# Kernel tuning notes

Hardware: AMD Instinct MI355X
Metric: run time of the kernel (lower is better)

## Reference

```python
import jax, jax.numpy as jnp
import numpy as np

B, L, DN, DE, DD, H = 2, 512, 512, 128, 128, 8
DK, DEH, DDH = DN // H, DE // H, DD // H
F = 2 * DK + DEH + 2 * DDH  # per-head concat feature size (176)
SLOPE = 0.2


def _kaiming(key, out_f, in_f):
    bound = np.sqrt(6.0 / ((1.0 + SLOPE ** 2) * in_f))
    return jax.random.uniform(key, (out_f, in_f), minval=-bound, maxval=bound, dtype=jnp.float32)


def lin(x, w, b):
    y = jnp.einsum('...i,oi->...o', x, w)
    return y if b is None else y + b


def setup_inputs() -> dict:
    key = jax.random.key(0)
    ks = jax.random.split(key, 16)
    inp = {
        'node_representation': jax.random.normal(ks[0], (B, L, DN), dtype=jnp.float32),
        'edge_representation': jax.random.normal(ks[1], (B, L, L, DE), dtype=jnp.float32),
        'diff_vec': jax.random.normal(ks[2], (B, L, DD), dtype=jnp.float32),
        'Wn_w': _kaiming(ks[3], DN, DN), 'Wn_b': jnp.zeros((DN,), jnp.float32),
        'We_w': _kaiming(ks[4], DE, DE), 'We_b': jnp.zeros((DE,), jnp.float32),
        'Wd_w': _kaiming(ks[5], DD, DD), 'Wd_b': jnp.zeros((DD,), jnp.float32),
        'Wh_w': _kaiming(ks[6], DK, DK), 'Wh_b': jnp.zeros((DK,), jnp.float32),
        'attn_w': _kaiming(ks[7], 1, F),
        'outn_w': _kaiming(ks[8], DN, DN), 'outn_b': jnp.zeros((DN,), jnp.float32),
        'Wn2_w': _kaiming(ks[9], DN, DN), 'Wn2_b': jnp.zeros((DN,), jnp.float32),
        'We2_w': _kaiming(ks[10], DE, DE), 'We2_b': jnp.zeros((DE,), jnp.float32),
        'Wd2_w': _kaiming(ks[11], DD, DD), 'Wd2_b': jnp.zeros((DD,), jnp.float32),
        'edge_w': _kaiming(ks[12], DEH, F), 'edge_b': jnp.zeros((DEH,), jnp.float32),
        'oute_w': _kaiming(ks[13], DE, DE), 'oute_b': jnp.zeros((DE,), jnp.float32),
    }
    return inp


def reference(node_representation, edge_representation, diff_vec,
              Wn_w, Wn_b, We_w, We_b, Wd_w, Wd_b, Wh_w, Wh_b, attn_w,
              outn_w, outn_b, Wn2_w, Wn2_b, We2_w, We2_b, Wd2_w, Wd2_b,
              edge_w, edge_b, oute_w, oute_b):
    lrelu = lambda x: jax.nn.leaky_relu(x, SLOPE)

    # ---- node update (GAT-style with concat score decomposed per term) ----
    npj = lin(node_representation, Wn_w, Wn_b).reshape(B, L, H, DK)
    epj = lin(edge_representation, We_w, We_b).reshape(B, L, L, H, DEH)
    dpj = lin(diff_vec, Wd_w, Wd_b).reshape(B, L, H, DDH)
    a = attn_w[0]  # concat order: [hi, hj, edge, di, dj]
    a_hi, a_hj = a[:DK], a[DK:2 * DK]
    a_e = a[2 * DK:2 * DK + DEH]
    a_di, a_dj = a[2 * DK + DEH:2 * DK + DEH + DDH], a[-DDH:]
    # scores[b,i,j,h]
    s = (jnp.einsum('blhd,d->blh', npj, a_hi)[:, :, None, :]
         + jnp.einsum('blhd,d->blh', npj, a_hj)[:, None, :, :]
         + jnp.einsum('blmhe,e->blmh', epj, a_e)
         + jnp.einsum('blhd,d->blh', dpj, a_di)[:, :, None, :]
         + jnp.einsum('blhd,d->blh', dpj, a_dj)[:, None, :, :])
    diag = jnp.eye(L, dtype=bool)[None, :, :, None]
    s = jnp.where(diag, -jnp.inf, s)
    probs = jax.nn.softmax(lrelu(s), axis=2)  # softmax over j
    node_wh = lin(npj, Wh_w, Wh_b)  # [B,L,H,DK]
    agg = jnp.einsum('blmh,bmhd->blhd', probs, node_wh)
    new_node = (npj + lrelu(agg)).reshape(B, L, DN)
    new_node = lin(new_node, outn_w, outn_b)

    # ---- edge update (concat-linear decomposed into per-term matmuls) ----
    np2 = lin(new_node, Wn2_w, Wn2_b).reshape(B, L, H, DK)
    ep2 = lin(edge_representation, We2_w, We2_b).reshape(B, L, L, H, DEH)
    dp2 = lin(diff_vec, Wd2_w, Wd2_b).reshape(B, L, H, DDH)
    # edge concat order: [edge, hi, hj, di, dj]
    W_e = edge_w[:, :DEH]
    W_hi = edge_w[:, DEH:DEH + DK]
    W_hj = edge_w[:, DEH + DK:DEH + 2 * DK]
    W_di = edge_w[:, DEH + 2 * DK:DEH + 2 * DK + DDH]
    W_dj = edge_w[:, -DDH:]
    e_out = (jnp.einsum('blmhe,fe->blmhf', ep2, W_e)
             + jnp.einsum('blhd,fd->blhf', np2, W_hi)[:, :, None]
             + jnp.einsum('blhd,fd->blhf', np2, W_hj)[:, None]
             + jnp.einsum('blhd,fd->blhf', dp2, W_di)[:, :, None]
             + jnp.einsum('blhd,fd->blhf', dp2, W_dj)[:, None]
             + edge_b)
    new_edge = lin(e_out.reshape(B, L, L, DE), oute_w, oute_b)
    return new_node, new_edge
```

## Files before the change

kernel.cpp:

```cpp
#include <hip/hip_runtime.h>
#include <hip/hip_bf16.h>

typedef unsigned short u16;
typedef unsigned short u16x8 __attribute__((ext_vector_type(8)));
typedef __bf16 bf16x8 __attribute__((ext_vector_type(8)));
typedef float f32x4 __attribute__((ext_vector_type(4)));

#define LRS 0.2f

__device__ __forceinline__ u16 f2b(float f) {
  __hip_bfloat16 h = __float2bfloat16(f);
  return __builtin_bit_cast(u16, h);
}

template<int K, int O, int KSEG, int R>
__device__ __forceinline__ void gemm_rowsR(const float* xr, const float* W, const float* bias,
                                           float* yl, float* yg, int ygstride) {
  constexpr int KPT = K / KSEG;
  constexpr int OPP = 256 / KSEG;
  const int t = threadIdx.x;
  const int ks = t % KSEG;
  const int oi = t / KSEG;
#pragma unroll
  for (int pass = 0; pass < O / OPP; ++pass) {
    const int o = pass * OPP + oi;
    float a[R];
#pragma unroll
    for (int r = 0; r < R; ++r) a[r] = 0.0f;
    const float* wp = W + (size_t)o * K + ks * KPT;
    const float* xb = xr + ks * KPT;
#pragma unroll 4
    for (int kc = 0; kc < KPT; kc += 4) {
      f32x4 w4 = *(const f32x4*)(wp + kc);
#pragma unroll
      for (int r = 0; r < R; ++r) {
        f32x4 x = *(const f32x4*)(xb + r * K + kc);
#pragma unroll
        for (int j = 0; j < 4; ++j) a[r] += x[j] * w4[j];
      }
    }
#pragma unroll
    for (int d = 1; d < KSEG; d <<= 1)
#pragma unroll
      for (int r = 0; r < R; ++r) a[r] += __shfl_xor(a[r], d, 64);
    if (ks == 0) {
      float bv = bias ? bias[o] : 0.0f;
#pragma unroll
      for (int r = 0; r < R; ++r) {
        float v = a[r] + bv;
        if (yl) yl[r * O + o] = v;
        if (yg) yg[(size_t)r * ygstride + o] = v;
      }
    }
  }
}

__global__ __launch_bounds__(256) void kW1(const float* We_w, const float* We_b, const float* attn,
                                           const float* We2_w, const float* We2_b,
                                           const float* edge_w, const float* edge_b,
                                           float* Mfull, u16* vb, float* cbe, float* sconst) {
  int gid = blockIdx.x * 256 + threadIdx.x;
  if (gid < 16384) {
    int hf = gid >> 7, c = gid & 127;
    int h = hf >> 4, fo = hf & 15;
    float s = 0;
    for (int e = 0; e < 16; ++e)
      s += edge_w[fo * 176 + e] * We2_w[(h * 16 + e) * 128 + c];
    Mfull[hf * 128 + c] = s;
  } else if (gid < 16384 + 2048) {
    int idx = gid - 16384;
    int c = idx >> 4, hc = idx & 15;
    float s = 0;
    if (hc < 8)
      for (int e = 0; e < 16; ++e)
        s += We_w[(hc * 16 + e) * 128 + c] * attn[128 + e];
    vb[c * 16 + hc] = f2b(s);
  } else if (gid < 18432 + 128) {
    int hf = gid - 18432;
    int h = hf >> 4, fo = hf & 15;
    float s = edge_b[fo];
    for (int e = 0; e < 16; ++e)
      s += We2_b[h * 16 + e] * edge_w[fo * 176 + e];
    cbe[hf] = s;
  } else if (gid < 18560 + 8) {
    int h = gid - 18560;
    float s = 0;
    for (int e = 0; e < 16; ++e)
      s += We_b[h * 16 + e] * attn[128 + e];
    sconst[h] = s;
  }
}

__global__ __launch_bounds__(256) void kW2(const float* oute_w, const float* Mfull, u16* Gb) {
  int gid = blockIdx.x * 256 + threadIdx.x;
  int o = gid >> 7, c = gid & 127;
  float s = 0;
  for (int k = 0; k < 128; ++k)
    s += oute_w[o * 128 + k] * Mfull[k * 128 + c];
  Gb[o * 128 + c] = f2b(s);
}

__global__ __launch_bounds__(256) void kN1(const float* node, const float* diff,
                                           const float* Wn_w, const float* Wn_b,
                                           const float* Wd_w, const float* Wd_b,
                                           const float* Wh_w, const float* Wh_b,
                                           const float* attn, const float* sconst,
                                           float* npj_g, float* nwh_g,
                                           float* srow_g, float* scol_g) {
  __shared__ float nrow[2 * 512], npjl[2 * 512], drow[2 * 128], dpjl[2 * 128];
  const int t = threadIdx.x;
  const int r0 = blockIdx.x * 2;
  *(f32x4*)&nrow[t * 4] = *(const f32x4*)(node + (size_t)r0 * 512 + t * 4);
  if (t < 64) *(f32x4*)&drow[t * 4] = *(const f32x4*)(diff + (size_t)r0 * 128 + t * 4);
  __syncthreads();
  gemm_rowsR<512, 512, 4, 2>(nrow, Wn_w, Wn_b, npjl, npj_g + (size_t)r0 * 512, 512);
  gemm_rowsR<128, 128, 4, 2>(drow, Wd_w, Wd_b, dpjl, nullptr, 0);
  __syncthreads();
  {
    int d = t & 63, hh = t >> 6;
#pragma unroll
    for (int hi = 0; hi < 2; ++hi) {
      int h = hh + hi * 4;
      float wb = Wh_b[d];
      float acc[2] = {wb, wb};
      for (int k = 0; k < 64; ++k) {
        float w = Wh_w[d * 64 + k];
#pragma unroll
        for (int r = 0; r < 2; ++r) acc[r] += npjl[r * 512 + h * 64 + k] * w;
      }
#pragma unroll
      for (int r = 0; r < 2; ++r) nwh_g[(size_t)(r0 + r) * 512 + h * 64 + d] = acc[r];
    }
  }
  if (t < 16) {
    int r = t >> 3, h = t & 7;
    float shi = 0, shj = 0, sdi = 0, sdj = 0;
    for (int d = 0; d < 64; ++d) {
      float x = npjl[r * 512 + h * 64 + d];
      shi += x * attn[d];
      shj += x * attn[64 + d];
    }
    for (int e = 0; e < 16; ++e) {
      float x = dpjl[r * 128 + h * 16 + e];
      sdi += x * attn[144 + e];
      sdj += x * attn[160 + e];
    }
    srow_g[(r0 + r) * 8 + h] = shi + sdi + sconst[h];
    scol_g[(r0 + r) * 8 + h] = shj + sdj;
  }
}

__global__ __launch_bounds__(256) void kA(const float* edge, const float* npj, const float* nwh,
                                          const float* srow, const float* scol,
                                          const u16* vb, float* nnp, u16* abf) {
  __shared__ u16 At[8192];
  __shared__ float sm[4608];
  __shared__ float part[2][512];
  __shared__ float red[256];
  __shared__ float mxh8[8], inv8[8];
  const int bl = blockIdx.x;
  const int b = bl >> 9, l = bl & 511;
  const int t = threadIdx.x;
  const int lane = t & 63, w = t >> 6;
  const int colL = lane & 15, kg = lane >> 4;
  const int h = t & 7, seg = t >> 3;
  const int arow = t >> 2, aseg = t & 3;

  bf16x8 bfr[4];
#pragma unroll
  for (int ks = 0; ks < 4; ++ks) {
    u16x8 u;
#pragma unroll
    for (int j = 0; j < 8; ++j) u[j] = vb[(ks * 32 + kg * 8 + j) * 16 + colL];
    bfr[ks] = __builtin_bit_cast(bf16x8, u);
  }

  for (int tl = 0; tl < 8; ++tl) {
    {
      const float* p = edge + ((size_t)bl * 512 + tl * 64 + arow) * 128 + aseg * 32;
      f32x4 v[8];
#pragma unroll
      for (int q = 0; q < 8; ++q) v[q] = *(const f32x4*)(p + q * 4);
      u16* dst = abf ? abf + ((size_t)bl * 8 + tl) * 8192 : nullptr;
#pragma unroll
      for (int jj = 0; jj < 4; ++jj) {
        u16x8 a8;
#pragma unroll
        for (int j2 = 0; j2 < 4; ++j2) {
          a8[j2]     = f2b(v[2 * jj][j2]);
          a8[4 + j2] = f2b(v[2 * jj + 1][j2]);
        }
        int cu = aseg * 4 + jj;
        int su = arow * 16 + (cu ^ (arow & 7));
        *(u16x8*)(At + su * 8) = a8;
        if (dst) *(u16x8*)(dst + su * 8) = a8;
      }
    }
    __syncthreads();
    f32x4 acc = {0, 0, 0, 0};
#pragma unroll
    for (int ks = 0; ks < 4; ++ks) {
      int cu = ks * 4 + kg;
      int lrow = w * 16 + colL;
      bf16x8 af = *(bf16x8*)(At + (lrow * 16 + (cu ^ (lrow & 7))) * 8);
      acc = __builtin_amdgcn_mfma_f32_16x16x32_bf16(af, bfr[ks], acc, 0, 0, 0);
    }
    if (colL < 8) {
#pragma unroll
      for (int r = 0; r < 4; ++r) {
        int m = tl * 64 + w * 16 + kg * 4 + r;
        sm[m * 9 + colL] = acc[r];
      }
    }
    __syncthreads();
  }

  const float srh2 = srow[(size_t)bl * 8 + h];
  float mx = -__builtin_inff();
#pragma unroll 4
  for (int i = 0; i < 16; ++i) {
    int m = seg * 16 + i;
    float sv = sm[m * 9 + h] + srh2 + scol[((size_t)b * 512 + m) * 8 + h];
    sv = (m == l) ? -__builtin_inff() : (sv >= 0.0f ? sv : LRS * sv);
    sm[m * 9 + h] = sv;
    mx = fmaxf(mx, sv);
  }
  red[t] = mx;
  __syncthreads();
  if (t < 8) {
    float m2 = -__builtin_inff();
    for (int sg = 0; sg < 32; ++sg) m2 = fmaxf(m2, red[sg * 8 + t]);
    mxh8[t] = m2;
  }
  __syncthreads();
  float mh = mxh8[h];
  float smv = 0;
#pragma unroll 4
  for (int i = 0; i < 16; ++i) {
    int m = seg * 16 + i;
    float p = __expf(sm[m * 9 + h] - mh);
    sm[m * 9 + h] = p;
    smv += p;
  }
  red[t] = smv;
  __syncthreads();
  if (t < 8) {
    float s2 = 0;
    for (int sg = 0; sg < 32; ++sg) s2 += red[sg * 8 + t];
    inv8[t] = 1.0f / s2;
  }
  __syncthreads();
  const int half = t >> 7, oq = t & 127;
  const int o4 = oq * 4, hh = oq >> 4;
  f32x4 acc4a = {0, 0, 0, 0}, acc4b = {0, 0, 0, 0};
  const float* nb = nwh + (size_t)b * 512 * 512;
  for (int m = half * 256; m < half * 256 + 256; m += 2) {
    acc4a += sm[m * 9 + hh]       * *(const f32x4*)(nb + (size_t)m * 512 + o4);
    acc4b += sm[(m + 1) * 9 + hh] * *(const f32x4*)(nb + (size_t)(m + 1) * 512 + o4);
  }
  *(f32x4*)&part[half][o4] = acc4a + acc4b;
  __syncthreads();
  if (t < 128) {
    int ob = t * 4, h2 = t >> 4;
    f32x4 s0 = *(f32x4*)&part[0][ob];
    f32x4 s1 = *(f32x4*)&part[1][ob];
    f32x4 np4 = *(const f32x4*)(npj + (size_t)bl * 512 + ob);
    float iv = inv8[h2];
    f32x4 o;
#pragma unroll
    for (int j = 0; j < 4; ++j) {
      float a = (s0[j] + s1[j]) * iv;
      a = a >= 0.0f ? a : LRS * a;
      o[j] = np4[j] + a;
    }
    *(f32x4*)(nnp + (size_t)bl * 512 + ob) = o;
  }
}

__global__ __launch_bounds__(256) void kN234(const float* nnp, const float* diff,
                                             const float* outn_w, const float* outn_b,
                                             const float* Wn2_w, const float* Wn2_b,
                                             const float* Wd2_w, const float* Wd2_b,
                                             const float* edge_w, const float* cbe,
                                             const float* oute_w, const float* oute_b,
                                             float* out0, float* Pl, float* Pm) {
  __shared__ float xr[2 * 512], o0l[2 * 512], np2l[2 * 512], dr[2 * 128], dp2l[2 * 128];
  __shared__ float Rls[2 * 128], Rms[2 * 128];
  const int t = threadIdx.x;
  const int r0 = blockIdx.x * 2;
  *(f32x4*)&xr[t * 4] = *(const f32x4*)(nnp + (size_t)r0 * 512 + t * 4);
  if (t < 64) *(f32x4*)&dr[t * 4] = *(const f32x4*)(diff + (size_t)r0 * 128 + t * 4);
  __syncthreads();
  gemm_rowsR<512, 512, 4, 2>(xr, outn_w, outn_b, o0l, out0 + (size_t)r0 * 512, 512);
  gemm_rowsR<128, 128, 4, 2>(dr, Wd2_w, Wd2_b, dp2l, nullptr, 0);
  __syncthreads();
  gemm_rowsR<512, 512, 4, 2>(o0l, Wn2_w, Wn2_b, np2l, nullptr, 0);
  __syncthreads();
  {
    int hf = t & 127, which = t >> 7;
    int h = hf >> 4, fo = hf & 15;
    const float* wh = edge_w + fo * 176 + 16 + which * 64;
    const float* wd = edge_w + fo * 176 + 144 + which * 16;
    float add = which ? 0.0f : cbe[hf];
    float* dst = which ? Rms : Rls;
#pragma unroll
    for (int r = 0; r < 2; ++r) {
      float a = add;
      for (int d = 0; d < 64; ++d) a += np2l[r * 512 + h * 64 + d] * wh[d];
      for (int e = 0; e < 16; ++e) a += dp2l[r * 128 + h * 16 + e] * wd[e];
      dst[r * 128 + hf] = a;
    }
  }
  __syncthreads();
  gemm_rowsR<128, 128, 4, 2>(Rls, oute_w, oute_b, nullptr, Pl + (size_t)r0 * 128, 128);
  gemm_rowsR<128, 128, 4, 2>(Rms, oute_w, nullptr, nullptr, Pm + (size_t)r0 * 128, 128);
}

__global__ __launch_bounds__(256) void kEc(const u16* Abf, const u16* Gb,
                                           const float* Pl, const float* Pm, float* oute) {
  __shared__ u16 Gt[16384];
  __shared__ u16 At[8192];
  const int tile = blockIdx.x;
  const int bl = tile >> 2;
  const int b = bl >> 9;
  const int q0 = (tile & 3) * 128;
  const int t = threadIdx.x, lane = t & 63, w = t >> 6;
#pragma unroll
  for (int i2 = 0; i2 < 8; ++i2) {
    int u = i2 * 256 + t;
    int row = u >> 4, cu = u & 15;
    *(u16x8*)(Gt + (row * 16 + (cu ^ (row & 7))) * 8) = *(const u16x8*)(Gb + u * 8);
  }
  const int wr = w >> 1, wc = w & 1;
  const int colL = lane & 15, kg = lane >> 4;
  const float* plp = Pl + (size_t)bl * 128;
  f32x4 plv4[4];
#pragma unroll
  for (int n = 0; n < 4; ++n) plv4[n] = *(const f32x4*)(plp + wc * 64 + n * 16 + kg * 4);

  for (int sub = 0; sub < 2; ++sub) {
    const int r0 = q0 + sub * 64;
    const int gs = (tile & 3) * 2 + sub;
    const u16* src = Abf + ((size_t)bl * 8 + gs) * 8192;
#pragma unroll
    for (int q = 0; q < 4; ++q)
      *(u16x8*)(At + q * 2048 + t * 8) = *(const u16x8*)(src + q * 2048 + t * 8);
    __syncthreads();
    f32x4 acc[2][4] = {};
#pragma unroll
    for (int ks = 0; ks < 4; ++ks) {
      int cu = ks * 4 + kg;
      bf16x8 af[2], bfv[4];
#pragma unroll
      for (int i = 0; i < 2; ++i) {
        int row = wr * 32 + i * 16 + colL;
        af[i] = *(bf16x8*)(At + (row * 16 + (cu ^ (row & 7))) * 8);
      }
#pragma unroll
      for (int n = 0; n < 4; ++n) {
        int orow = wc * 64 + n * 16 + colL;
        bfv[n] = *(bf16x8*)(Gt + (orow * 16 + (cu ^ (orow & 7))) * 8);
      }
#pragma unroll
      for (int i = 0; i < 2; ++i)
#pragma unroll
        for (int n = 0; n < 4; ++n)
          acc[i][n] = __builtin_amdgcn_mfma_f32_16x16x32_bf16(bfv[n], af[i], acc[i][n], 0, 0, 0);
    }
    float* ob = oute + ((size_t)bl * 512 + r0) * 128;
#pragma unroll
    for (int i = 0; i < 2; ++i) {
      int m = wr * 32 + i * 16 + colL;
      const float* pmp = Pm + ((size_t)b * 512 + r0 + m) * 128;
      float* orow = ob + (size_t)m * 128;
#pragma unroll
      for (int n = 0; n < 4; ++n) {
        int oc = wc * 64 + n * 16 + kg * 4;
        f32x4 pm4 = *(const f32x4*)(pmp + oc);
        f32x4 o4;
#pragma unroll
        for (int r = 0; r < 4; ++r) o4[r] = acc[i][n][r] + plv4[n][r] + pm4[r];
        *(f32x4*)(orow + oc) = o4;
      }
    }
    __syncthreads();
  }
}

__global__ __launch_bounds__(256) void kEd(const float* edge, const u16* Gb,
                                           const float* Pl, const float* Pm, float* oute) {
  __shared__ u16 Gt[16384];
  __shared__ u16 At[8192];
  const int tile = blockIdx.x;
  const int bl = tile >> 2;
  const int b = bl >> 9;
  const int q0 = (tile & 3) * 128;
  const int t = threadIdx.x, lane = t & 63, w = t >> 6;
#pragma unroll
  for (int i2 = 0; i2 < 8; ++i2) {
    int u = i2 * 256 + t;
    int row = u >> 4, cu = u & 15;
    *(u16x8*)(Gt + (row * 16 + (cu ^ (row & 7))) * 8) = *(const u16x8*)(Gb + u * 8);
  }
  const int wr = w >> 1, wc = w & 1;
  const int colL = lane & 15, kg = lane >> 4;
  const float* plp = Pl + (size_t)bl * 128;
  f32x4 plv4[4];
#pragma unroll
  for (int n = 0; n < 4; ++n) plv4[n] = *(const f32x4*)(plp + wc * 64 + n * 16 + kg * 4);
  const int arow = t >> 2, aseg = t & 3;

  for (int sub = 0; sub < 2; ++sub) {
    const int r0 = q0 + sub * 64;
    {
      const float* p = edge + ((size_t)bl * 512 + r0 + arow) * 128 + aseg * 32;
      f32x4 v[8];
#pragma unroll
      for (int q = 0; q < 8; ++q) v[q] = *(const f32x4*)(p + q * 4);
#pragma unroll
      for (int jj = 0; jj < 4; ++jj) {
        u16x8 a8;
#pragma unroll
        for (int j2 = 0; j2 < 4; ++j2) {
          a8[j2]     = f2b(v[2 * jj][j2]);
          a8[4 + j2] = f2b(v[2 * jj + 1][j2]);
        }
        int cu = aseg * 4 + jj;
        *(u16x8*)(At + (arow * 16 + (cu ^ (arow & 7))) * 8) = a8;
      }
    }
    __syncthreads();
    f32x4 acc[2][4] = {};
#pragma unroll
    for (int ks = 0; ks < 4; ++ks) {
      int cu = ks * 4 + kg;
      bf16x8 af[2], bfv[4];
#pragma unroll
      for (int i = 0; i < 2; ++i) {
        int row = wr * 32 + i * 16 + colL;
        af[i] = *(bf16x8*)(At + (row * 16 + (cu ^ (row & 7))) * 8);
      }
#pragma unroll
      for (int n = 0; n < 4; ++n) {
        int orow = wc * 64 + n * 16 + colL;
        bfv[n] = *(bf16x8*)(Gt + (orow * 16 + (cu ^ (orow & 7))) * 8);
      }
#pragma unroll
      for (int i = 0; i < 2; ++i)
#pragma unroll
        for (int n = 0; n < 4; ++n)
          acc[i][n] = __builtin_amdgcn_mfma_f32_16x16x32_bf16(bfv[n], af[i], acc[i][n], 0, 0, 0);
    }
    float* ob = oute + ((size_t)bl * 512 + r0) * 128;
#pragma unroll
    for (int i = 0; i < 2; ++i) {
      int m = wr * 32 + i * 16 + colL;
      const float* pmp = Pm + ((size_t)b * 512 + r0 + m) * 128;
      float* orow = ob + (size_t)m * 128;
#pragma unroll
      for (int n = 0; n < 4; ++n) {
        int oc = wc * 64 + n * 16 + kg * 4;
        f32x4 pm4 = *(const f32x4*)(pmp + oc);
        f32x4 o4;
#pragma unroll
        for (int r = 0; r < 4; ++r) o4[r] = acc[i][n][r] + plv4[n][r] + pm4[r];
        *(f32x4*)(orow + oc) = o4;
      }
    }
    __syncthreads();
  }
}

extern "C" void kernel_launch(void* const* d_in, const int* in_sizes, int n_in,
                              void* d_out, int out_size, void* d_ws, size_t ws_size,
                              hipStream_t stream) {
  (void)in_sizes; (void)n_in; (void)out_size;
  const float* node   = (const float*)d_in[0];
  const float* edge   = (const float*)d_in[1];
  const float* diff   = (const float*)d_in[2];
  const float* Wn_w   = (const float*)d_in[3];
  const float* Wn_b   = (const float*)d_in[4];
  const float* We_w   = (const float*)d_in[5];
  const float* We_b   = (const float*)d_in[6];
  const float* Wd_w   = (const float*)d_in[7];
  const float* Wd_b   = (const float*)d_in[8];
  const float* Wh_w   = (const float*)d_in[9];
  const float* Wh_b   = (const float*)d_in[10];
  const float* attn   = (const float*)d_in[11];
  const float* outn_w = (const float*)d_in[12];
  const float* outn_b = (const float*)d_in[13];
  const float* Wn2_w  = (const float*)d_in[14];
  const float* Wn2_b  = (const float*)d_in[15];
  const float* We2_w  = (const float*)d_in[16];
  const float* We2_b  = (const float*)d_in[17];
  const float* Wd2_w  = (const float*)d_in[18];
  const float* Wd2_b  = (const float*)d_in[19];
  const float* edge_w = (const float*)d_in[20];
  const float* edge_b = (const float*)d_in[21];
  const float* oute_w = (const float*)d_in[22];
  const float* oute_b = (const float*)d_in[23];

  float* out0 = (float*)d_out;
  float* out1 = out0 + 524288;

  float* f = (float*)d_ws;
  size_t off = 0;
  auto alloc = [&](size_t n) { float* p = f + off; off += (n + 7) & ~(size_t)7; return p; };
  float* npj    = alloc(524288);
  float* nwh    = alloc(524288);
  float* srow   = alloc(8192);
  float* scol   = alloc(8192);
  float* sconst = alloc(8);
  float* cbe    = alloc(128);
  float* Mfull  = alloc(16384);
  float* nnp    = alloc(524288);
  float* Pl     = alloc(131072);
  float* Pm     = alloc(131072);
  u16* vb = (u16*)(f + off); off += 1024;
  u16* Gb = (u16*)(f + off); off += 8192;
  const size_t abf_elems = (size_t)2 * 512 * 512 * 128;
  bool cache = ws_size >= off * 4 + abf_elems * 2 + 256;
  u16* Abf = cache ? (u16*)(f + off) : nullptr;

  hipLaunchKernelGGL(kW1, dim3(73), dim3(256), 0, stream,
                     We_w, We_b, attn, We2_w, We2_b, edge_w, edge_b, Mfull, vb, cbe, sconst);
  hipLaunchKernelGGL(kW2, dim3(64), dim3(256), 0, stream, oute_w, Mfull, Gb);
  hipLaunchKernelGGL(kN1, dim3(512), dim3(256), 0, stream,
                     node, diff, Wn_w, Wn_b, Wd_w, Wd_b, Wh_w, Wh_b, attn, sconst,
                     npj, nwh, srow, scol);
  hipLaunchKernelGGL(kA, dim3(1024), dim3(256), 0, stream,
                     edge, npj, nwh, srow, scol, vb, nnp, Abf);
  hipLaunchKernelGGL(kN234, dim3(512), dim3(256), 0, stream,
                     nnp, diff, outn_w, outn_b, Wn2_w, Wn2_b, Wd2_w, Wd2_b,
                     edge_w, cbe, oute_w, oute_b, out0, Pl, Pm);
  if (cache)
    hipLaunchKernelGGL(kEc, dim3(4096), dim3(256), 0, stream, Abf, Gb, Pl, Pm, out1);
  else
    hipLaunchKernelGGL(kEd, dim3(4096), dim3(256), 0, stream, edge, Gb, Pl, Pm, out1);
}
```

Measured before the change: 474.5 us.

## Split attention aggregation into a separate bf16 MFMA kernel and pipeline edge loads

kA no longer aggregates probs·node_wh per row. It now writes unnormalized bf16 probabilities and per-head inverse sums to workspace, and a new kAgg kernel does the aggregation as a batched bf16 MFMA GEMM over 64-row tiles. This removes the per-row reread of the 1 MB nwh matrix, which was streamed by every block. kA also double-buffers its LDS tile, prefetches the next edge chunk into registers, and changes the cached bf16 layout to unswizzled, with kEc swizzling on load. The cost is an extra launch, a 2 MB workspace round trip for P, and bf16 rounding of both the probabilities and nwh in the aggregation.

```diff
diff --git a/kernel.cpp b/kernel.cpp
--- a/kernel.cpp
+++ b/kernel.cpp
@@ -150,21 +150,18 @@
   }
 }
 
-__global__ __launch_bounds__(256) void kA(const float* edge, const float* npj, const float* nwh,
-                                          const float* srow, const float* scol,
-                                          const u16* vb, float* nnp, u16* abf) {
-  __shared__ u16 At[8192];
-  __shared__ float sm[4608];
-  __shared__ float part[2][512];
+__global__ __launch_bounds__(256) void kA(const float* edge, const float* srow, const float* scol,
+                                          const u16* vb, u16* P, float* invs, u16* abf) {
+  __shared__ u16 At[2][8192];
+  __shared__ float smx[512 * 9];
   __shared__ float red[256];
-  __shared__ float mxh8[8], inv8[8];
+  __shared__ float mxh8[8];
   const int bl = blockIdx.x;
   const int b = bl >> 9, l = bl & 511;
   const int t = threadIdx.x;
   const int lane = t & 63, w = t >> 6;
   const int colL = lane & 15, kg = lane >> 4;
   const int h = t & 7, seg = t >> 3;
-  const int arow = t >> 2, aseg = t & 3;
 
   bf16x8 bfr[4];
 #pragma unroll
@@ -175,25 +172,32 @@
     bfr[ks] = __builtin_bit_cast(bf16x8, u);
   }
 
+  const float* eb = edge + (size_t)bl * 65536;
+  f32x4 va[8], vn[8];
+#pragma unroll
+  for (int j = 0; j < 4; ++j) {
+    va[2 * j]     = *(const f32x4*)(eb + j * 2048 + t * 8);
+    va[2 * j + 1] = *(const f32x4*)(eb + j * 2048 + t * 8 + 4);
+  }
   for (int tl = 0; tl < 8; ++tl) {
-    {
-      const float* p = edge + ((size_t)bl * 512 + tl * 64 + arow) * 128 + aseg * 32;
-      f32x4 v[8];
-#pragma unroll
-      for (int q = 0; q < 8; ++q) v[q] = *(const f32x4*)(p + q * 4);
-      u16* dst = abf ? abf + ((size_t)bl * 8 + tl) * 8192 : nullptr;
-#pragma unroll
-      for (int jj = 0; jj < 4; ++jj) {
-        u16x8 a8;
-#pragma unroll
-        for (int j2 = 0; j2 < 4; ++j2) {
-          a8[j2]     = f2b(v[2 * jj][j2]);
-          a8[4 + j2] = f2b(v[2 * jj + 1][j2]);
-        }
-        int cu = aseg * 4 + jj;
-        int su = arow * 16 + (cu ^ (arow & 7));
-        *(u16x8*)(At + su * 8) = a8;
-        if (dst) *(u16x8*)(dst + su * 8) = a8;
+    u16* cdst = abf ? abf + ((size_t)bl * 8 + tl) * 8192 : nullptr;
+    u16* lbuf = At[tl & 1];
+#pragma unroll
+    for (int j = 0; j < 4; ++j) {
+      u16x8 a8;
+#pragma unroll
+      for (int q = 0; q < 4; ++q) { a8[q] = f2b(va[2 * j][q]); a8[4 + q] = f2b(va[2 * j + 1][q]); }
+      int c = j * 256 + t;
+      int row = c >> 4, cu = c & 15;
+      *(u16x8*)(lbuf + (row * 16 + (cu ^ (row & 7))) * 8) = a8;
+      if (cdst) *(u16x8*)(cdst + c * 8) = a8;
+    }
+    if (tl < 7) {
+      const float* nb2 = eb + (tl + 1) * 8192;
+#pragma unroll
+      for (int j = 0; j < 4; ++j) {
+        vn[2 * j]     = *(const f32x4*)(nb2 + j * 2048 + t * 8);
+        vn[2 * j + 1] = *(const f32x4*)(nb2 + j * 2048 + t * 8 + 4);
       }
     }
     __syncthreads();
@@ -202,27 +206,27 @@
     for (int ks = 0; ks < 4; ++ks) {
       int cu = ks * 4 + kg;
       int lrow = w * 16 + colL;
-      bf16x8 af = *(bf16x8*)(At + (lrow * 16 + (cu ^ (lrow & 7))) * 8);
+      bf16x8 af = *(bf16x8*)(lbuf + (lrow * 16 + (cu ^ (lrow & 7))) * 8);
       acc = __builtin_amdgcn_mfma_f32_16x16x32_bf16(af, bfr[ks], acc, 0, 0, 0);
     }
     if (colL < 8) {
 #pragma unroll
-      for (int r = 0; r < 4; ++r) {
-        int m = tl * 64 + w * 16 + kg * 4 + r;
-        sm[m * 9 + colL] = acc[r];
-      }
-    }
-    __syncthreads();
-  }
+      for (int r = 0; r < 4; ++r)
+        smx[(tl * 64 + w * 16 + kg * 4 + r) * 9 + colL] = acc[r];
+    }
+#pragma unroll
+    for (int q = 0; q < 8; ++q) va[q] = vn[q];
+  }
+  __syncthreads();
 
   const float srh2 = srow[(size_t)bl * 8 + h];
   float mx = -__builtin_inff();
 #pragma unroll 4
   for (int i = 0; i < 16; ++i) {
     int m = seg * 16 + i;
-    float sv = sm[m * 9 + h] + srh2 + scol[((size_t)b * 512 + m) * 8 + h];
+    float sv = smx[m * 9 + h] + srh2 + scol[((size_t)b * 512 + m) * 8 + h];
     sv = (m == l) ? -__builtin_inff() : (sv >= 0.0f ? sv : LRS * sv);
-    sm[m * 9 + h] = sv;
+    smx[m * 9 + h] = sv;
     mx = fmaxf(mx, sv);
   }
   red[t] = mx;
@@ -238,8 +242,8 @@
 #pragma unroll 4
   for (int i = 0; i < 16; ++i) {
     int m = seg * 16 + i;
-    float p = __expf(sm[m * 9 + h] - mh);
-    sm[m * 9 + h] = p;
+    float p = __expf(smx[m * 9 + h] - mh);
+    smx[m * 9 + h] = p;
     smv += p;
   }
   red[t] = smv;
@@ -247,33 +251,78 @@
   if (t < 8) {
     float s2 = 0;
     for (int sg = 0; sg < 32; ++sg) s2 += red[sg * 8 + t];
-    inv8[t] = 1.0f / s2;
-  }
-  __syncthreads();
-  const int half = t >> 7, oq = t & 127;
-  const int o4 = oq * 4, hh = oq >> 4;
-  f32x4 acc4a = {0, 0, 0, 0}, acc4b = {0, 0, 0, 0};
-  const float* nb = nwh + (size_t)b * 512 * 512;
-  for (int m = half * 256; m < half * 256 + 256; m += 2) {
-    acc4a += sm[m * 9 + hh]       * *(const f32x4*)(nb + (size_t)m * 512 + o4);
-    acc4b += sm[(m + 1) * 9 + hh] * *(const f32x4*)(nb + (size_t)(m + 1) * 512 + o4);
-  }
-  *(f32x4*)&part[half][o4] = acc4a + acc4b;
-  __syncthreads();
-  if (t < 128) {
-    int ob = t * 4, h2 = t >> 4;
-    f32x4 s0 = *(f32x4*)&part[0][ob];
-    f32x4 s1 = *(f32x4*)&part[1][ob];
-    f32x4 np4 = *(const f32x4*)(npj + (size_t)bl * 512 + ob);
-    float iv = inv8[h2];
-    f32x4 o;
-#pragma unroll
-    for (int j = 0; j < 4; ++j) {
-      float a = (s0[j] + s1[j]) * iv;
+    invs[(size_t)bl * 8 + t] = 1.0f / s2;
+  }
+  __syncthreads();
+#pragma unroll
+  for (int k = 0; k < 2; ++k) {
+    int c = k * 256 + t;
+    int hp = c >> 6, mb = (c & 63) * 8;
+    u16x8 pk;
+#pragma unroll
+    for (int j = 0; j < 8; ++j) pk[j] = f2b(smx[(mb + j) * 9 + hp]);
+    *(u16x8*)(P + (((size_t)b * 8 + hp) * 512 + l) * 512 + mb) = pk;
+  }
+}
+
+__global__ __launch_bounds__(256) void kAgg(const u16* P, const float* nwh, const float* npj,
+                                            const float* invs, float* nnp) {
+  __shared__ u16 Pt[8192];
+  __shared__ u16 Vt[8192];
+  const int bid = blockIdx.x;
+  const int lt = bid & 7, h = (bid >> 3) & 7, b = bid >> 6;
+  const int l0 = lt * 64;
+  const int t = threadIdx.x;
+  const int lane = t & 63, w = t >> 6;
+  const int colL = lane & 15, kg = lane >> 4;
+
+  f32x4 acc[4] = {};
+  for (int mc = 0; mc < 4; ++mc) {
+#pragma unroll
+    for (int q = 0; q < 4; ++q) {
+      int c = q * 256 + t;
+      int row = c >> 4, cu = c & 15;
+      u16x8 a8 = *(const u16x8*)(P + (((size_t)b * 8 + h) * 512 + l0 + row) * 512 + mc * 128 + cu * 8);
+      *(u16x8*)(Pt + (row * 16 + (cu ^ (row & 7))) * 8) = a8;
+    }
+#pragma unroll
+    for (int q = 0; q < 8; ++q) {
+      int c = q * 256 + t;
+      int m = c >> 4, d4 = (c & 15) * 4;
+      f32x4 v = *(const f32x4*)(nwh + ((size_t)b * 512 + mc * 128 + m) * 512 + h * 64 + d4);
+#pragma unroll
+      for (int j = 0; j < 4; ++j) {
+        int d = d4 + j;
+        Vt[(d * 16 + ((m >> 3) ^ (d & 7))) * 8 + (m & 7)] = f2b(v[j]);
+      }
+    }
+    __syncthreads();
+#pragma unroll
+    for (int kc = 0; kc < 4; ++kc) {
+      int cu = kc * 4 + kg;
+      int prow = w * 16 + colL;
+      bf16x8 af = *(bf16x8*)(Pt + (prow * 16 + (cu ^ (prow & 7))) * 8);
+#pragma unroll
+      for (int n = 0; n < 4; ++n) {
+        int d = n * 16 + colL;
+        bf16x8 bf = *(bf16x8*)(Vt + (d * 16 + (cu ^ (d & 7))) * 8);
+        acc[n] = __builtin_amdgcn_mfma_f32_16x16x32_bf16(af, bf, acc[n], 0, 0, 0);
+      }
+    }
+    __syncthreads();
+  }
+#pragma unroll
+  for (int r = 0; r < 4; ++r) {
+    int l = l0 + w * 16 + kg * 4 + r;
+    float iv = invs[((size_t)b * 512 + l) * 8 + h];
+#pragma unroll
+    for (int n = 0; n < 4; ++n) {
+      int o = h * 64 + n * 16 + colL;
+      size_t idx = ((size_t)b * 512 + l) * 512 + o;
+      float a = acc[n][r] * iv;
       a = a >= 0.0f ? a : LRS * a;
-      o[j] = np4[j] + a;
-    }
-    *(f32x4*)(nnp + (size_t)bl * 512 + ob) = o;
+      nnp[idx] = npj[idx] + a;
+    }
   }
 }
 
@@ -343,8 +392,12 @@
     const int gs = (tile & 3) * 2 + sub;
     const u16* src = Abf + ((size_t)bl * 8 + gs) * 8192;
 #pragma unroll
-    for (int q = 0; q < 4; ++q)
-      *(u16x8*)(At + q * 2048 + t * 8) = *(const u16x8*)(src + q * 2048 + t * 8);
+    for (int q = 0; q < 4; ++q) {
+      int c = q * 256 + t;
+      u16x8 a8 = *(const u16x8*)(src + c * 8);
+      int row = c >> 4, cu = c & 15;
+      *(u16x8*)(At + (row * 16 + (cu ^ (row & 7))) * 8) = a8;
+    }
     __syncthreads();
     f32x4 acc[2][4] = {};
 #pragma unroll
@@ -516,8 +569,10 @@
   float* nnp    = alloc(524288);
   float* Pl     = alloc(131072);
   float* Pm     = alloc(131072);
+  float* invs   = alloc(8192);
   u16* vb = (u16*)(f + off); off += 1024;
   u16* Gb = (u16*)(f + off); off += 8192;
+  u16* P  = (u16*)(f + off); off += 2097152;
   const size_t abf_elems = (size_t)2 * 512 * 512 * 128;
   bool cache = ws_size >= off * 4 + abf_elems * 2 + 256;
   u16* Abf = cache ? (u16*)(f + off) : nullptr;
@@ -529,7 +584,8 @@
                      node, diff, Wn_w, Wn_b, Wd_w, Wd_b, Wh_w, Wh_b, attn, sconst,
                      npj, nwh, srow, scol);
   hipLaunchKernelGGL(kA, dim3(1024), dim3(256), 0, stream,
-                     edge, npj, nwh, srow, scol, vb, nnp, Abf);
+                     edge, srow, scol, vb, P, invs, Abf);
+  hipLaunchKernelGGL(kAgg, dim3(128), dim3(256), 0, stream, P, nwh, npj, invs, nnp);
   hipLaunchKernelGGL(kN234, dim3(512), dim3(256), 0, stream,
                      nnp, diff, outn_w, outn_b, Wn2_w, Wn2_b, Wd2_w, Wd2_b,
                      edge_w, cbe, oute_w, oute_b, out0, Pl, Pm);
```

New measurement: 460.1 us. 3.0% less time.
